# Optimization experiments

Measured on AMD Instinct MI355X. Metric: run time of the kernel, lower is better.

## Reference

```python
import jax, jax.numpy as jnp
import numpy as np

N_EMBD = 2048
N_Q = 32
N_KV = 8
GROUP = N_Q // N_KV   # 4
HD = N_EMBD // N_Q    # 64
BASE = 10000.0
NEG_INF = -1e30


def _rope(x):
    """Rotate-half RoPE on last dim; positions 1..t along dim -2 (as in the
    original _build_cache which uses arange(1, seq_len+1))."""
    t, d = x.shape[-2], x.shape[-1]
    d2 = d // 2
    theta = 1.0 / (BASE ** (jnp.arange(0, d, 2, dtype=jnp.float32) / d))  # (d/2,)
    pos = jnp.arange(1, t + 1, dtype=jnp.float32)                          # (t,)
    ang = pos[:, None] * theta[None, :]                                    # (t, d/2)
    ang = jnp.concatenate([ang, ang], axis=-1)                             # (t, d)
    sin, cos = jnp.sin(ang), jnp.cos(ang)
    rot = jnp.concatenate([-x[..., d2:], x[..., :d2]], axis=-1)
    return x * cos + rot * sin


def setup_inputs() -> dict:
    key = jax.random.key(0)
    ks = jax.random.split(key, 5)
    b, t = 2, 1024
    s = 1.0 / np.sqrt(N_EMBD)
    return {
        "x": jax.random.normal(ks[0], (b, t, N_EMBD), dtype=jnp.float32),
        "wq": jax.random.normal(ks[1], (N_EMBD, N_EMBD), dtype=jnp.float32) * s,
        "bq": jnp.zeros((N_EMBD,), dtype=jnp.float32),
        "wk": jax.random.normal(ks[2], (N_EMBD, N_KV * HD), dtype=jnp.float32) * s,
        "bk": jnp.zeros((N_KV * HD,), dtype=jnp.float32),
        "wv": jax.random.normal(ks[3], (N_EMBD, N_KV * HD), dtype=jnp.float32) * s,
        "bv": jnp.zeros((N_KV * HD,), dtype=jnp.float32),
        "wo": jax.random.normal(ks[4], (N_EMBD, N_EMBD), dtype=jnp.float32) * s,
        "bo": jnp.zeros((N_EMBD,), dtype=jnp.float32),
    }


def reference(x, wq, bq, wk, bk, wv, bv, wo, bo):
    b, t, _ = x.shape
    q = x @ wq + bq                                   # (b, t, E)
    k = x @ wk + bk                                   # (b, t, NKV*HD)
    v = x @ wv + bv
    q = q.reshape(b, t, N_Q, HD).transpose(0, 2, 1, 3)        # (b, nq, t, d)
    q = q.reshape(b, N_KV, GROUP, t, HD)                      # (b, hkv, g, t, d)
    k = k.reshape(b, t, N_KV, HD).transpose(0, 2, 1, 3)       # (b, hkv, t, d)
    v = v.reshape(b, t, N_KV, HD).transpose(0, 2, 1, 3)
    q = _rope(q)
    k = _rope(k)
    scale = jnp.sqrt(jnp.float32(HD))
    att = jnp.einsum("bhgqd,bhkd->bhgqk", q, k) / scale       # (b, hkv, g, t, t)
    causal = jnp.tril(jnp.ones((t, t), dtype=bool))
    att = jnp.where(causal, att, NEG_INF)
    att = jax.nn.softmax(att, axis=-1)
    out = jnp.einsum("bhgqk,bhkd->bhgqd", att, v)             # (b, hkv, g, t, d)
    out = out.transpose(0, 3, 1, 2, 4).reshape(b, t, N_EMBD)  # (b, t, E)
    return out @ wo + bo
```

## Files before the change

kernel.cpp:

```cpp
#include <hip/hip_runtime.h>
#include <hip/hip_bf16.h>
#include <cstdint>


typedef __attribute__((ext_vector_type(8))) short short8;
typedef __attribute__((ext_vector_type(4))) short short4v;
typedef __attribute__((ext_vector_type(4))) float f32x4;

__device__ inline short f2b(float f) {
  union { float f; unsigned u; } v; v.f = f;
  unsigned r = v.u + 0x7fffu + ((v.u >> 16) & 1u);
  return (short)(r >> 16);
}

__device__ inline float exp2_fast(float x) {
  float r;
  asm("v_exp_f32 %0, %1" : "=v"(r) : "v"(x));
  return r;
}

__device__ inline void gl_lds16(const void* g, void* l) {
  __builtin_amdgcn_global_load_lds((const __attribute__((address_space(1))) void*)g,
                                   (__attribute__((address_space(3))) void*)l,
                                   16, 0, 0);
}

__global__ void prep_all(const float* __restrict__ x, const float* __restrict__ wq,
                         const float* __restrict__ wk, const float* __restrict__ wv,
                         const float* __restrict__ wo, short* __restrict__ xb,
                         short* __restrict__ WqkvT, short* __restrict__ woT, int n4) {
  __shared__ float tile[64][65];
  const int bx = blockIdx.x;
  const int tid = threadIdx.x;
  if (bx >= 80) {
    int i = ((bx - 80) * 32 + blockIdx.y) * 256 + tid;
    if (i < n4) {
      float4 v = ((const float4*)x)[i];
      short4v o; o.x = f2b(v.x); o.y = f2b(v.y); o.z = f2b(v.z); o.w = f2b(v.w);
      ((short4v*)xb)[i] = o;
    }
    return;
  }
  const float* W; short* WT; int N, off, nb;
  if (bx < 32)      { W = wq; WT = WqkvT; N = 2048; off = 0;    nb = bx * 64; }
  else if (bx < 40) { W = wk; WT = WqkvT; N = 512;  off = 2048; nb = (bx - 32) * 64; }
  else if (bx < 48) { W = wv; WT = WqkvT; N = 512;  off = 2560; nb = (bx - 40) * 64; }
  else              { W = wo; WT = woT;   N = 2048; off = 0;    nb = (bx - 48) * 64; }
  const int kb = blockIdx.y * 64;
  const int c = tid & 63, r0 = tid >> 6;
#pragma unroll
  for (int s = 0; s < 16; ++s) {
    int k = r0 + s * 4;
    tile[c][k] = W[(size_t)(kb + k) * N + nb + c];
  }
  __syncthreads();
#pragma unroll
  for (int s = 0; s < 16; ++s) {
    int n = r0 + s * 4;
    WT[(size_t)(off + nb + n) * 2048 + kb + c] = f2b(tile[n][c]);
  }
}

__device__ __forceinline__ void gemm_loop_bk64(const short* __restrict__ Ag,
                                               const short* __restrict__ Bg,
                                               short* lA, short* lB,
                                               int w, int l15, int q4,
                                               f32x4 acc[2][4]) {
  const int K = 2048, NS = 32;
  const int q4x = q4 ^ ((l15 >> 1) & 3);
  auto stage = [&](int s, int d) {
    const short* As = Ag + s * 64;
    const short* Bs = Bg + s * 64;
    short* a = lA + d * 8192 + w * 512;
    gl_lds16(As, a);
    gl_lds16(As + 64 * K, a + 2048);
    gl_lds16(As + 32, a + 4096);
    gl_lds16(As + 64 * K + 32, a + 6144);
    short* bp = lB + d * 4096 + w * 512;
    gl_lds16(Bs, bp);
    gl_lds16(Bs + 32, bp + 2048);
  };
  stage(0, 0);
  for (int s = 0; s < NS; ++s) {
    const int d = s & 1;
    __syncthreads();
    if (s + 1 < NS) stage(s + 1, d ^ 1);
#pragma unroll
    for (int ks = 0; ks < 2; ++ks) {
      const short* ap = lA + d * 8192 + ks * 4096;
      const short* bp = lB + d * 4096 + ks * 2048;
      short8 af[2], bf[4];
#pragma unroll
      for (int mf = 0; mf < 2; ++mf) af[mf] = *(const short8*)(ap + (w * 32 + mf * 16 + l15) * 32 + q4x * 8);
#pragma unroll
      for (int nf = 0; nf < 4; ++nf) bf[nf] = *(const short8*)(bp + (nf * 16 + l15) * 32 + q4x * 8);
#pragma unroll
      for (int mf = 0; mf < 2; ++mf)
#pragma unroll
        for (int nf = 0; nf < 4; ++nf)
          acc[mf][nf] = __builtin_amdgcn_mfma_f32_16x16x32_bf16(af[mf], bf[nf], acc[mf][nf], 0, 0, 0);
    }
  }
}

__launch_bounds__(256, 3)
__global__ void gemm_qkv(const short* __restrict__ A, const short* __restrict__ BT,
                         const float* __restrict__ bq, const float* __restrict__ bk,
                         const float* __restrict__ bv,
                         short* __restrict__ Qb, short* __restrict__ Kb,
                         short* __restrict__ VTb) {
  __shared__ __align__(16) short lA[16384];
  __shared__ __align__(16) short lB[8192];
  const int K = 2048;
  const int tid = threadIdx.x, lane = tid & 63, w = tid >> 6;
  const int q4 = lane >> 4, l15 = lane & 15;
  const int bn = blockIdx.x * 64, bm = blockIdx.y * 128;

  const int swzc = ((tid & 3) ^ ((tid >> 3) & 3)) << 3;
  const short* Ag = A + (size_t)(bm + (tid >> 2)) * K + swzc;
  const short* Bg = BT + (size_t)(bn + (tid >> 2)) * K + swzc;

  f32x4 acc[2][4];
  const f32x4 fz = {0.f, 0.f, 0.f, 0.f};
#pragma unroll
  for (int i = 0; i < 2; ++i)
#pragma unroll
    for (int j = 0; j < 4; ++j) acc[i][j] = fz;

  gemm_loop_bk64(Ag, Bg, lA, lB, w, l15, q4, acc);

  const float L2T = 0.4152410118609203f;
  const float theta_a = exp2_fast(-(float)l15 * L2T);
  const float theta_b = exp2_fast(-(float)(l15 + 16) * L2T);
  const float s2 = 0.18033688011112042f;

  if (bn < 2048) {
    const int h = bn >> 6;
    float bb0 = bq[bn + l15], bb1 = bq[bn + 16 + l15], bb2 = bq[bn + 32 + l15], bb3 = bq[bn + 48 + l15];
#pragma unroll
    for (int mf = 0; mf < 2; ++mf)
#pragma unroll
      for (int r = 0; r < 4; ++r) {
        int row = bm + w * 32 + mf * 16 + q4 * 4 + r;
        int batch = row >> 10, t = row & 1023;
        float pos = (float)(t + 1);
        float sa, ca, sb, cb;
        __sincosf(pos * theta_a, &sa, &ca);
        __sincosf(pos * theta_b, &sb, &cb);
        float x0 = acc[mf][0][r] + bb0, x2 = acc[mf][2][r] + bb2;
        float x1 = acc[mf][1][r] + bb1, x3 = acc[mf][3][r] + bb3;
        size_t base = ((size_t)(batch * 32 + h) * 1024 + t) * 64;
        Qb[base + l15]      = f2b((x0 * ca - x2 * sa) * s2);
        Qb[base + l15 + 32] = f2b((x2 * ca + x0 * sa) * s2);
        Qb[base + l15 + 16] = f2b((x1 * cb - x3 * sb) * s2);
        Qb[base + l15 + 48] = f2b((x3 * cb + x1 * sb) * s2);
      }
  } else if (bn < 2560) {
    const int co = bn - 2048;
    const int hkv = co >> 6;
    float bb0 = bk[co + l15], bb1 = bk[co + 16 + l15], bb2 = bk[co + 32 + l15], bb3 = bk[co + 48 + l15];
#pragma unroll
    for (int mf = 0; mf < 2; ++mf)
#pragma unroll
      for (int r = 0; r < 4; ++r) {
        int row = bm + w * 32 + mf * 16 + q4 * 4 + r;
        int batch = row >> 10, t = row & 1023;
        float pos = (float)(t + 1);
        float sa, ca, sb, cb;
        __sincosf(pos * theta_a, &sa, &ca);
        __sincosf(pos * theta_b, &sb, &cb);
        float x0 = acc[mf][0][r] + bb0, x2 = acc[mf][2][r] + bb2;
        float x1 = acc[mf][1][r] + bb1, x3 = acc[mf][3][r] + bb3;
        size_t base = (size_t)(batch * 8 + hkv) * 65536 + t * 32;
        Kb[base + l15]              = f2b(x0 * ca - x2 * sa);
        Kb[base + l15 + 16]         = f2b(x1 * cb - x3 * sb);
        Kb[base + 32768 + l15]      = f2b(x2 * ca + x0 * sa);
        Kb[base + 32768 + l15 + 16] = f2b(x3 * cb + x1 * sb);
      }
  } else {
    const int co = bn - 2560;
    const int hkv = co >> 6;
    float bb[4];
#pragma unroll
    for (int nf = 0; nf < 4; ++nf) bb[nf] = bv[co + nf * 16 + l15];
    const int batch = (bm + w * 32) >> 10;
    const size_t vbase = (size_t)(batch * 8 + hkv) * 65536;
#pragma unroll
    for (int mf = 0; mf < 2; ++mf) {
      const int t0 = (bm + w * 32 + mf * 16 + q4 * 4) & 1023;
      const size_t rbase = vbase + (size_t)(t0 >> 5) * 2048 + (t0 & 31);
#pragma unroll
      for (int nf = 0; nf < 4; ++nf) {
        short4v pk;
#pragma unroll
        for (int r = 0; r < 4; ++r) pk[r] = f2b(acc[mf][nf][r] + bb[nf]);
        *(short4v*)(VTb + rbase + (nf * 16 + l15) * 32) = pk;
      }
    }
  }
}

#define PROW 72
__launch_bounds__(256, 3)
__global__ void attn9_kernel(const short* __restrict__ Qb, const short* __restrict__ Kb,
                             const short* __restrict__ VTb, short* __restrict__ AO) {
  __shared__ __align__(16) short lK[2 * 4096];
  __shared__ __align__(16) short lVT[2 * 4096];
  __shared__ __align__(16) short lP[4][16 * PROW];
  const int tid = threadIdx.x, lane = tid & 63, w = tid >> 6;
  const int q4 = lane >> 4, l15 = lane & 15;
  const int q4x = q4 ^ ((l15 >> 1) & 3);
  const int swzc = ((tid & 3) ^ ((tid >> 3) & 3)) << 3;
  const int pr = blockIdx.x;
  const int jA = pr, jB = 15 - pr;
  const int h = blockIdx.y, b = blockIdx.z;
  const int hkv = h >> 2;

  const short* Qg = Qb + (size_t)(b * 32 + h) * 65536;
  const short* Kg = Kb + (size_t)(b * 8 + hkv) * 65536;
  const short* Vg = VTb + (size_t)(b * 8 + hkv) * 65536;

  short8 qfA0, qfA1, qfB0, qfB1;
  {
    const short* qr = Qg + (size_t)(jA * 64 + w * 16 + l15) * 64 + q4 * 8;
    qfA0 = *(const short8*)(qr); qfA1 = *(const short8*)(qr + 32);
    const short* qr2 = Qg + (size_t)(jB * 64 + w * 16 + l15) * 64 + q4 * 8;
    qfB0 = *(const short8*)(qr2); qfB1 = *(const short8*)(qr2 + 32);
  }

  const f32x4 fz = {0.f, 0.f, 0.f, 0.f};
  f32x4 o[4], ol;
  short8 ones;
#pragma unroll
  for (int i = 0; i < 8; ++i) ones[i] = (short)0x3F80;

  auto stage = [&](int kt, int d) {
    const short* Ksrc = Kg + (size_t)(kt * 64 + (tid >> 2)) * 32 + swzc;
    short* kd = lK + d * 4096 + w * 512;
    gl_lds16(Ksrc, kd);
    gl_lds16(Ksrc + 32768, kd + 2048);
    const short* Vsrc = Vg + (size_t)(2 * kt) * 2048 + (tid >> 2) * 32 + swzc;
    short* vd = lVT + d * 4096 + w * 512;
    gl_lds16(Vsrc, vd);
    gl_lds16(Vsrc + 2048, vd + 2048);
  };

  auto comp = [&](int d, int kt, int jt, short8 qf0, short8 qf1) {
    const short* kp = lK + d * 4096;
    const short* vp = lVT + d * 4096;
    short8 kf0[4], kf1[4];
#pragma unroll
    for (int nt = 0; nt < 4; ++nt) {
      kf0[nt] = *(const short8*)(kp + (nt * 16 + l15) * 32 + q4x * 8);
      kf1[nt] = *(const short8*)(kp + 2048 + (nt * 16 + l15) * 32 + q4x * 8);
    }
    f32x4 sv[4];
#pragma unroll
    for (int nt = 0; nt < 4; ++nt) {
      f32x4 z = __builtin_amdgcn_mfma_f32_16x16x32_bf16(qf0, kf0[nt], fz, 0, 0, 0);
      sv[nt] = __builtin_amdgcn_mfma_f32_16x16x32_bf16(qf1, kf1[nt], z, 0, 0, 0);
    }
    if (kt == jt) {
#pragma unroll
      for (int r = 0; r < 4; ++r) {
        const int qrow = jt * 64 + w * 16 + q4 * 4 + r;
        const int col = kt * 64 + l15;
#pragma unroll
        for (int nt = 0; nt < 4; ++nt)
          if (col + nt * 16 > qrow) sv[nt][r] = -1e30f;
      }
    }
    short* lPm = lP[w];
#pragma unroll
    for (int r = 0; r < 4; ++r)
#pragma unroll
      for (int nt = 0; nt < 4; ++nt)
        lPm[(q4 * 4 + r) * PROW + nt * 16 + l15] = f2b(exp2_fast(sv[nt][r] - 16.f));
    short8 vf0[4], vf1[4];
#pragma unroll
    for (int dt = 0; dt < 4; ++dt) {
      vf0[dt] = *(const short8*)(vp + (dt * 16 + l15) * 32 + q4x * 8);
      vf1[dt] = *(const short8*)(vp + 2048 + (dt * 16 + l15) * 32 + q4x * 8);
    }
    short8 pf0 = *(const short8*)(lPm + l15 * PROW + q4 * 8);
    short8 pf1 = *(const short8*)(lPm + l15 * PROW + 32 + q4 * 8);
    ol = __builtin_amdgcn_mfma_f32_16x16x32_bf16(pf0, ones, ol, 0, 0, 0);
    ol = __builtin_amdgcn_mfma_f32_16x16x32_bf16(pf1, ones, ol, 0, 0, 0);
#pragma unroll
    for (int dt = 0; dt < 4; ++dt) {
      o[dt] = __builtin_amdgcn_mfma_f32_16x16x32_bf16(pf0, vf0[dt], o[dt], 0, 0, 0);
      o[dt] = __builtin_amdgcn_mfma_f32_16x16x32_bf16(pf1, vf1[dt], o[dt], 0, 0, 0);
    }
  };

  auto emit = [&](int jt) {
#pragma unroll
    for (int r = 0; r < 4; ++r) {
      float inv = __builtin_amdgcn_rcpf(ol[r]);
      int row = jt * 64 + w * 16 + q4 * 4 + r;
#pragma unroll
      for (int dt = 0; dt < 4; ++dt)
        AO[(size_t)(b * 1024 + row) * 2048 + h * 64 + dt * 16 + l15] = f2b(o[dt][r] * inv);
    }
  };

  ol = fz;
#pragma unroll
  for (int dt = 0; dt < 4; ++dt) o[dt] = fz;

  const int nsA = jA + 1;
  stage(0, 0);
  for (int s = 0; s < 17; ++s) {
    const int d = s & 1;
    __syncthreads();
    if (s + 1 < 17) stage((s + 1 < nsA) ? s + 1 : s + 1 - nsA, d ^ 1);
    if (s < nsA) {
      comp(d, s, jA, qfA0, qfA1);
    } else {
      if (s == nsA) {
        emit(jA);
        ol = fz;
#pragma unroll
        for (int dt = 0; dt < 4; ++dt) o[dt] = fz;
      }
      comp(d, s - nsA, jB, qfB0, qfB1);
    }
  }
  emit(jB);
}

__launch_bounds__(256, 3)
__global__ void gemm_out(const short* __restrict__ A, const short* __restrict__ BT,
                         float* __restrict__ C, const float* __restrict__ bias,
                         int N, int K) {
  __shared__ __align__(16) short lA[16384];
  __shared__ __align__(16) short lB[8192];
  const int tid = threadIdx.x, lane = tid & 63, w = tid >> 6;
  const int q4 = lane >> 4, l15 = lane & 15;
  const int bn = blockIdx.x * 64, bm = blockIdx.y * 128;

  const int swzc = ((tid & 3) ^ ((tid >> 3) & 3)) << 3;
  const short* Ag = A + (size_t)(bm + (tid >> 2)) * K + swzc;
  const short* Bg = BT + (size_t)(bn + (tid >> 2)) * K + swzc;

  f32x4 acc[2][4];
  const f32x4 fz = {0.f, 0.f, 0.f, 0.f};
#pragma unroll
  for (int i = 0; i < 2; ++i)
#pragma unroll
    for (int j = 0; j < 4; ++j) acc[i][j] = fz;

  gemm_loop_bk64(Ag, Bg, lA, lB, w, l15, q4, acc);

#pragma unroll
  for (int mf = 0; mf < 2; ++mf)
#pragma unroll
    for (int nf = 0; nf < 4; ++nf) {
      int col = bn + nf * 16 + l15;
      float bb = bias[col];
#pragma unroll
      for (int r = 0; r < 4; ++r) {
        int row = bm + w * 32 + mf * 16 + q4 * 4 + r;
        C[(size_t)row * N + col] = acc[mf][nf][r] + bb;
      }
    }
}

extern "C" void kernel_launch(void* const* d_in, const int* in_sizes, int n_in,
                              void* d_out, int out_size, void* d_ws, size_t ws_size,
                              hipStream_t stream) {
  const float* x  = (const float*)d_in[0];
  const float* wq = (const float*)d_in[1];
  const float* bq = (const float*)d_in[2];
  const float* wk = (const float*)d_in[3];
  const float* bk = (const float*)d_in[4];
  const float* wv = (const float*)d_in[5];
  const float* bv = (const float*)d_in[6];
  const float* wo = (const float*)d_in[7];
  const float* bo = (const float*)d_in[8];
  float* out = (float*)d_out;
  const int B = in_sizes[0] / (1024 * 2048);
  const int M = B * 1024;

  char* ws = (char*)d_ws;
  size_t off = 0;
  auto alloc = [&](size_t bytes) -> char* {
    char* p = ws + off;
    off += (bytes + 255) & ~(size_t)255;
    return p;
  };
  short* xb    = (short*)alloc((size_t)M * 2048 * 2);
  short* WqkvT = (short*)alloc((size_t)3072 * 2048 * 2);
  short* woT   = (short*)alloc((size_t)2048 * 2048 * 2);
  short* Qb    = (short*)alloc((size_t)B * 32 * 1024 * 64 * 2);
  short* Kb    = (short*)alloc((size_t)B * 8 * 2 * 1024 * 32 * 2);
  short* VTb   = (short*)alloc((size_t)B * 8 * 32 * 64 * 32 * 2);
  short* AO    = (short*)alloc((size_t)M * 2048 * 2);

  const int n4 = M * 2048 / 4;
  const int nbc = (n4 + 255) / 256;
  prep_all<<<dim3(80 + (nbc + 31) / 32, 32), 256, 0, stream>>>(x, wq, wk, wv, wo, xb, WqkvT, woT, n4);
  gemm_qkv<<<dim3(48, M / 128), 256, 0, stream>>>(xb, WqkvT, bq, bk, bv, Qb, Kb, VTb);
  attn9_kernel<<<dim3(8, 32, B), 256, 0, stream>>>(Qb, Kb, VTb, AO);
  gemm_out<<<dim3(32, M / 128), 256, 0, stream>>>(AO, woT, out, bo, 2048, 2048);
}
```

Before: 196.6 us.

## Software-pipeline attention: overlap QK softmax of step s with PV of step s-1

```diff
diff --git a/kernel.cpp b/kernel.cpp
--- a/kernel.cpp
+++ b/kernel.cpp
@@ -201,18 +201,19 @@
 }
 
 #define PROW 72
-__launch_bounds__(256, 3)
-__global__ void attn9_kernel(const short* __restrict__ Qb, const short* __restrict__ Kb,
-                             const short* __restrict__ VTb, short* __restrict__ AO) {
+__launch_bounds__(256, 2)
+__global__ void attn10_kernel(const short* __restrict__ Qb, const short* __restrict__ Kb,
+                              const short* __restrict__ VTb, short* __restrict__ AO) {
   __shared__ __align__(16) short lK[2 * 4096];
-  __shared__ __align__(16) short lVT[2 * 4096];
-  __shared__ __align__(16) short lP[4][16 * PROW];
+  __shared__ __align__(16) short lV[3 * 4096];
+  __shared__ __align__(16) short lP[2][4][16 * PROW];
   const int tid = threadIdx.x, lane = tid & 63, w = tid >> 6;
   const int q4 = lane >> 4, l15 = lane & 15;
   const int q4x = q4 ^ ((l15 >> 1) & 3);
   const int swzc = ((tid & 3) ^ ((tid >> 3) & 3)) << 3;
   const int pr = blockIdx.x;
   const int jA = pr, jB = 15 - pr;
+  const int nsA = jA + 1;
   const int h = blockIdx.y, b = blockIdx.z;
   const int hkv = h >> 2;
 
@@ -233,21 +234,29 @@
   short8 ones;
 #pragma unroll
   for (int i = 0; i < 8; ++i) ones[i] = (short)0x3F80;
-
-  auto stage = [&](int kt, int d) {
+  ol = fz;
+#pragma unroll
+  for (int dt = 0; dt < 4; ++dt) o[dt] = fz;
+
+  auto stage = [&](int s) {
+    const int kt = (s < nsA) ? s : s - nsA;
     const short* Ksrc = Kg + (size_t)(kt * 64 + (tid >> 2)) * 32 + swzc;
-    short* kd = lK + d * 4096 + w * 512;
+    short* kd = lK + (s & 1) * 4096 + w * 512;
     gl_lds16(Ksrc, kd);
     gl_lds16(Ksrc + 32768, kd + 2048);
     const short* Vsrc = Vg + (size_t)(2 * kt) * 2048 + (tid >> 2) * 32 + swzc;
-    short* vd = lVT + d * 4096 + w * 512;
+    short* vd = lV + (s % 3) * 4096 + w * 512;
     gl_lds16(Vsrc, vd);
     gl_lds16(Vsrc + 2048, vd + 2048);
   };
 
-  auto comp = [&](int d, int kt, int jt, short8 qf0, short8 qf1) {
-    const short* kp = lK + d * 4096;
-    const short* vp = lVT + d * 4096;
+  auto qk = [&](int s) {
+    const int inA = (s < nsA);
+    const int jt = inA ? jA : jB;
+    const int kt = inA ? s : s - nsA;
+    const short8 qf0 = inA ? qfA0 : qfB0;
+    const short8 qf1 = inA ? qfA1 : qfB1;
+    const short* kp = lK + (s & 1) * 4096;
     short8 kf0[4], kf1[4];
 #pragma unroll
     for (int nt = 0; nt < 4; ++nt) {
@@ -270,12 +279,17 @@
           if (col + nt * 16 > qrow) sv[nt][r] = -1e30f;
       }
     }
-    short* lPm = lP[w];
+    short* lPm = lP[s & 1][w];
 #pragma unroll
     for (int r = 0; r < 4; ++r)
 #pragma unroll
       for (int nt = 0; nt < 4; ++nt)
         lPm[(q4 * 4 + r) * PROW + nt * 16 + l15] = f2b(exp2_fast(sv[nt][r] - 16.f));
+  };
+
+  auto pv = [&](int sp) {
+    const short* vp = lV + (sp % 3) * 4096;
+    const short* lPm = lP[sp & 1][w];
     short8 vf0[4], vf1[4];
 #pragma unroll
     for (int dt = 0; dt < 4; ++dt) {
@@ -304,28 +318,22 @@
     }
   };
 
-  ol = fz;
-#pragma unroll
-  for (int dt = 0; dt < 4; ++dt) o[dt] = fz;
-
-  const int nsA = jA + 1;
-  stage(0, 0);
+  stage(0);
   for (int s = 0; s < 17; ++s) {
-    const int d = s & 1;
     __syncthreads();
-    if (s + 1 < 17) stage((s + 1 < nsA) ? s + 1 : s + 1 - nsA, d ^ 1);
-    if (s < nsA) {
-      comp(d, s, jA, qfA0, qfA1);
-    } else {
-      if (s == nsA) {
+    if (s + 1 < 17) stage(s + 1);
+    qk(s);
+    if (s > 0) {
+      pv(s - 1);
+      if (s - 1 == nsA - 1) {
         emit(jA);
         ol = fz;
 #pragma unroll
         for (int dt = 0; dt < 4; ++dt) o[dt] = fz;
       }
-      comp(d, s - nsA, jB, qfB0, qfB1);
-    }
-  }
+    }
+  }
+  pv(16);
   emit(jB);
 }
 
@@ -401,6 +409,6 @@
   const int nbc = (n4 + 255) / 256;
   prep_all<<<dim3(80 + (nbc + 31) / 32, 32), 256, 0, stream>>>(x, wq, wk, wv, wo, xb, WqkvT, woT, n4);
   gemm_qkv<<<dim3(48, M / 128), 256, 0, stream>>>(xb, WqkvT, bq, bk, bv, Qb, Kb, VTb);
-  attn9_kernel<<<dim3(8, 32, B), 256, 0, stream>>>(Qb, Kb, VTb, AO);
+  attn10_kernel<<<dim3(8, 32, B), 256, 0, stream>>>(Qb, Kb, VTb, AO);
   gemm_out<<<dim3(32, M / 128), 256, 0, stream>>>(AO, woT, out, bo, 2048, 2048);
 }
```

Measured after the change: 196.3 us. No clear change (-0.2%).
